# Kernel optimization log

Hardware: AMD Instinct MI355X
Metric: run time of the kernel (lower is better)

Reference implementation:

```python
import jax, jax.numpy as jnp
import numpy as np

B, D = 16, 8192
CH = 32
N_BLOCKS = 24
DILATIONS = [2 ** i for i in range(8)] * 3  # 3 stacks of 8 layers


def _causal_conv(x, W, b, dilation):
    # x: (B, Cin, L); W: (Cout, Cin, K). Causal = left-pad (K-1)*dilation only,
    # which equals torch's symmetric-pad-then-slice-right trick.
    pad = (W.shape[-1] - 1) * dilation
    y = jax.lax.conv_general_dilated(
        x, W, window_strides=(1,), padding=[(pad, 0)],
        rhs_dilation=(dilation,), dimension_numbers=('NCH', 'OIH', 'NCH'))
    return y + b[None, :, None]


def setup_inputs() -> dict:
    key = jax.random.key(0)
    ks = jax.random.split(key, 13)
    s = 0.1  # keep activations in a sane range
    return {
        'x': jax.random.normal(ks[0], (B, D), jnp.float32),
        'W0': jax.random.normal(ks[1], (CH, 1, 2), jnp.float32) * s,
        'b0': jax.random.normal(ks[2], (CH,), jnp.float32) * s,
        'Wd': jax.random.normal(ks[3], (N_BLOCKS, 2 * CH, CH, 2), jnp.float32) * s,
        'bd': jax.random.normal(ks[4], (N_BLOCKS, 2 * CH), jnp.float32) * s,
        'W1': jax.random.normal(ks[5], (N_BLOCKS, CH, CH), jnp.float32) * s,
        'b1': jax.random.normal(ks[6], (N_BLOCKS, CH), jnp.float32) * s,
        'Wf': jax.random.normal(ks[7], (CH, CH), jnp.float32) * s,
        'bf': jax.random.normal(ks[8], (CH,), jnp.float32) * s,
        'fW1': jax.random.normal(ks[9], (64, CH * 4), jnp.float32) * s,
        'fb1': jax.random.normal(ks[10], (64,), jnp.float32) * s,
        'fW2': jax.random.normal(ks[11], (10, 64), jnp.float32) * s,
        'fb2': jax.random.normal(ks[12], (10,), jnp.float32) * s,
    }


def reference(x, W0, b0, Wd, bd, W1, b1, Wf, bf, fW1, fb1, fW2, fb2):
    h = _causal_conv(x[:, None, :], W0, b0, 1)  # (B, 32, L)
    skip_sum = jnp.zeros_like(h)
    for i, dil in enumerate(DILATIONS):
        z = _causal_conv(h, Wd[i], bd[i], dil)          # (B, 64, L)
        f, g = jnp.split(z, 2, axis=1)
        gated = jnp.tanh(f) * jax.nn.sigmoid(g)          # (B, 32, L)
        skip = jnp.einsum('oc,bcl->bol', W1[i], gated) + b1[i][None, :, None]
        h = h + skip                                     # residual (dropout = eval identity)
        skip_sum = skip_sum + skip                       # sum of stacked skips
    y = jax.nn.relu(skip_sum)
    y = jnp.einsum('oc,bcl->bol', Wf, y) + bf[None, :, None]
    y = jax.nn.relu(y)
    # AdaptiveMaxPool1d(4): L divisible by 4 -> max over contiguous chunks
    Bc, C, L = y.shape
    y = y.reshape(Bc, C, 4, L // 4).max(axis=-1)         # (B, 32, 4)
    y = y.reshape(Bc, C * 4)
    y = jax.nn.relu(y @ fW1.T + fb1)
    return y @ fW2.T + fb2
```

## Files before the change

kernel.cpp:

```cpp
#include <hip/hip_runtime.h>
#include <hip/hip_bf16.h>

#define BATCH 16
#define SEQ 8192
#define CH 32
#define NB 24

typedef __attribute__((ext_vector_type(8))) short short8;
typedef __attribute__((ext_vector_type(4))) short short4v;
typedef __attribute__((ext_vector_type(4))) float f32x4;

#define LROW 36

__device__ __forceinline__ unsigned short f2bf(float x) {
    __hip_bfloat16 b = __float2bfloat16(x);
    unsigned short u;
    __builtin_memcpy(&u, &b, 2);
    return u;
}
__device__ __forceinline__ float bf2f(unsigned short h) {
    return __uint_as_float(((unsigned int)h) << 16);
}
__device__ __forceinline__ float rcp_fast(float x) { return __builtin_amdgcn_rcpf(x); }

__device__ __forceinline__ float gate_fn(float f, float g) {
    float ef = __expf(-2.0f * fabsf(f));
    float eg = __expf(-g);
    float num = 1.0f - ef;
    float den = (1.0f + ef) * (1.0f + eg);
    return copysignf(num * rcp_fast(den), f);
}

__device__ __forceinline__ void split2(float v, unsigned short& h, unsigned short& l) {
    h = f2bf(v);
    l = f2bf(v - bf2f(h));
}

__global__ __launch_bounds__(64) void k_prep(const float* __restrict__ Wd,
                                             const float* __restrict__ bd,
                                             const float* __restrict__ W1,
                                             const float* __restrict__ b1,
                                             unsigned short* __restrict__ stream,
                                             float* __restrict__ pooled) {
    int i = blockIdx.x;
    int l = threadIdx.x;
    int p = l & 15, h4 = l >> 4;
    const float* wd  = Wd + (size_t)i * 64 * 64;
    const float* w1  = W1 + (size_t)i * 1024;
    const float* bdp = bd + (size_t)i * 64;
    const float* b1p = b1 + (size_t)i * 32;
    unsigned short* out = stream + (size_t)i * (28672 / 2);

    for (int g = blockIdx.x * 64 + l; g < BATCH * CH * 4; g += NB * 64)
        pooled[g] = 0.0f;

    for (int rt = 0; rt < 4; ++rt)
        for (int q = 0; q < 2; ++q) {
            int slot = rt * 2 + q;
            for (int j = 0; j < 8; ++j) {
                int m = 16 * rt + p;
                int k = 32 * q + 8 * h4 + j;
                int c = k & 31, tap = k >> 5;
                float w = wd[m * 64 + c * 2 + tap];
                unsigned short hi = f2bf(w);
                out[(size_t)slot * 512 + l * 8 + j] = hi;
                out[(size_t)(8 + slot) * 512 + l * 8 + j] = f2bf(w - bf2f(hi));
            }
        }
    for (int rt2 = 0; rt2 < 2; ++rt2)
        for (int j = 0; j < 8; ++j) {
            int o = 16 * rt2 + p, c = 8 * h4 + j;
            float w = w1[o * 32 + c];
            unsigned short hi = f2bf(w);
            out[(size_t)(16 + rt2) * 512 + l * 8 + j] = hi;
            out[(size_t)(18 + rt2) * 512 + l * 8 + j] = f2bf(w - bf2f(hi));
        }
    float* outf = (float*)stream + (size_t)i * (28672 / 4);
    for (int rt = 0; rt < 4; ++rt)
        for (int r = 0; r < 4; ++r)
            outf[(size_t)(20 + rt) * 256 + l * 4 + r] = bdp[16 * rt + 4 * h4 + r];
    for (int rt2 = 0; rt2 < 2; ++rt2)
        for (int r = 0; r < 4; ++r)
            outf[(size_t)(24 + rt2) * 256 + l * 4 + r] = b1p[16 * rt2 + 4 * h4 + r];
}

__global__ __launch_bounds__(512, 2) void k_stack(
        const float* __restrict__ hin,
        float* __restrict__ hout,
        const float* __restrict__ x,
        const float* __restrict__ W0,
        const float* __restrict__ b0,
        const float* __restrict__ Wf,
        const float* __restrict__ bf,
        float* __restrict__ pooled,
        const unsigned short* __restrict__ wstream,
        int stack) {
    __shared__ __align__(16) float lh[768 * LROW];
    __shared__ __align__(16) unsigned short gbuf[8][2][2][16][40];
    __shared__ float red[8 * CH];

    int tid = threadIdx.x;
    int lane = tid & 63, wave = tid >> 6;
    int p = lane & 15, h4 = lane >> 4;
    int bb = blockIdx.x >> 4;
    int T0 = (blockIdx.x & 15) * 512;
    bool first = (stack == 0);
    bool last  = (stack == 2);

    const float* pin = hin + (size_t)bb * SEQ * CH;
    float* pout = hout + (size_t)bb * SEQ * CH;
    const float* px = x + (size_t)bb * SEQ;

    const f32x4 zero4 = {0.0f, 0.0f, 0.0f, 0.0f};

    if (first) {
        for (int i = tid; i < 768; i += 512) {
            int t = T0 - 256 + i;
            float* dst = &lh[i * LROW];
            if (t >= 0) {
                float xt = px[t];
                float xm = (t > 0) ? px[t - 1] : 0.0f;
                __align__(16) float hv[CH];
#pragma unroll
                for (int c = 0; c < CH; ++c)
                    hv[c] = W0[c * 2] * xm + W0[c * 2 + 1] * xt + b0[c];
#pragma unroll
                for (int k = 0; k < 8; ++k)
                    *(f32x4*)(dst + 4 * k) = *(const f32x4*)(hv + 4 * k);
            } else {
#pragma unroll
                for (int k = 0; k < 8; ++k)
                    *(f32x4*)(dst + 4 * k) = zero4;
            }
        }
    } else {
        for (int i = tid; i < 768; i += 512) {
            int t = T0 - 256 + i;
            float* dst = &lh[i * LROW];
            if (t >= 0) {
                const float* src = pin + (size_t)t * CH;
#pragma unroll
                for (int k = 0; k < 8; ++k)
                    *(f32x4*)(dst + 4 * k) = *(const f32x4*)(src + 4 * k);
            } else {
#pragma unroll
                for (int k = 0; k < 8; ++k)
                    *(f32x4*)(dst + 4 * k) = zero4;
            }
        }
    }
    __syncthreads();

#pragma unroll 1
    for (int l = 0; l < 8; ++l) {
        int dil = 1 << l;
        const unsigned short* frag = wstream + (size_t)(8 * stack + l) * 14336;
        const short8* fs = (const short8*)frag;
        short8 Ah[4][2], Al[4][2], Sh[2], Sl[2];
#pragma unroll
        for (int rt = 0; rt < 4; ++rt)
#pragma unroll
            for (int q = 0; q < 2; ++q) {
                Ah[rt][q] = fs[(rt * 2 + q) * 64 + lane];
                Al[rt][q] = fs[(8 + rt * 2 + q) * 64 + lane];
            }
#pragma unroll
        for (int rt2 = 0; rt2 < 2; ++rt2) {
            Sh[rt2] = fs[(16 + rt2) * 64 + lane];
            Sl[rt2] = fs[(18 + rt2) * 64 + lane];
        }
        const f32x4* ff = (const f32x4*)frag;
        f32x4 bFG[4], bS[2];
#pragma unroll
        for (int rt = 0; rt < 4; ++rt) bFG[rt] = ff[(20 + rt) * 64 + lane];
#pragma unroll
        for (int rt2 = 0; rt2 < 2; ++rt2) bS[rt2] = ff[(24 + rt2) * 64 + lane];

        f32x4 hnew[6][2];

#pragma unroll
        for (int i = 0; i < 7; ++i) {
            f32x4 acc[4];
            if (i < 6) {
                int tpos = wave * 96 + i * 16 + p;
                int tq = tpos - dil;
                bool ok = (T0 - 256 + tq >= 0);
                int tqc = (tq > 0) ? tq : 0;

                const float* r1 = &lh[tpos * LROW + 8 * h4];
                const float* r0 = &lh[tqc * LROW + 8 * h4];
                f32x4 v1a = *(const f32x4*)r1, v1b = *(const f32x4*)(r1 + 4);
                f32x4 v0a = *(const f32x4*)r0, v0b = *(const f32x4*)(r0 + 4);
                if (!ok) { v0a = zero4; v0b = zero4; }
                short8 bh1, bl1, bh0, bl0;
#pragma unroll
                for (int j = 0; j < 4; ++j) {
                    unsigned short hh, ll;
                    split2(v1a[j], hh, ll); bh1[j] = (short)hh; bl1[j] = (short)ll;
                    split2(v1b[j], hh, ll); bh1[4 + j] = (short)hh; bl1[4 + j] = (short)ll;
                    split2(v0a[j], hh, ll); bh0[j] = (short)hh; bl0[j] = (short)ll;
                    split2(v0b[j], hh, ll); bh0[4 + j] = (short)hh; bl0[4 + j] = (short)ll;
                }
#pragma unroll
                for (int rt = 0; rt < 4; ++rt) {
                    f32x4 a = bFG[rt];
                    a = __builtin_amdgcn_mfma_f32_16x16x32_bf16(Ah[rt][0], bh0, a, 0, 0, 0);
                    a = __builtin_amdgcn_mfma_f32_16x16x32_bf16(Ah[rt][1], bh1, a, 0, 0, 0);
                    a = __builtin_amdgcn_mfma_f32_16x16x32_bf16(Ah[rt][0], bl0, a, 0, 0, 0);
                    a = __builtin_amdgcn_mfma_f32_16x16x32_bf16(Ah[rt][1], bl1, a, 0, 0, 0);
                    a = __builtin_amdgcn_mfma_f32_16x16x32_bf16(Al[rt][0], bh0, a, 0, 0, 0);
                    a = __builtin_amdgcn_mfma_f32_16x16x32_bf16(Al[rt][1], bh1, a, 0, 0, 0);
                    acc[rt] = a;
                }
            }

            if (i > 0) {
                asm volatile("s_waitcnt lgkmcnt(0)" ::: "memory");
                int ip = i - 1;
                int tposP = wave * 96 + ip * 16 + p;
                short8 Bgh = *(const short8*)&gbuf[wave][ip & 1][0][p][8 * h4];
                short8 Bgl = *(const short8*)&gbuf[wave][ip & 1][1][p][8 * h4];

                f32x4 sacc[2];
#pragma unroll
                for (int rt2 = 0; rt2 < 2; ++rt2) {
                    f32x4 a = bS[rt2];
                    a = __builtin_amdgcn_mfma_f32_16x16x32_bf16(Sh[rt2], Bgh, a, 0, 0, 0);
                    a = __builtin_amdgcn_mfma_f32_16x16x32_bf16(Sh[rt2], Bgl, a, 0, 0, 0);
                    a = __builtin_amdgcn_mfma_f32_16x16x32_bf16(Sl[rt2], Bgh, a, 0, 0, 0);
                    sacc[rt2] = a;
                }
#pragma unroll
                for (int rt2 = 0; rt2 < 2; ++rt2) {
                    f32x4 hold = *(const f32x4*)&lh[tposP * LROW + 16 * rt2 + 4 * h4];
                    hnew[ip][rt2] = hold + sacc[rt2];
                }
            }

            if (i < 6) {
#pragma unroll
                for (int rt = 0; rt < 2; ++rt) {
                    __align__(8) unsigned short g4h[4], g4l[4];
#pragma unroll
                    for (int r = 0; r < 4; ++r) {
                        float gated = gate_fn(acc[rt][r], acc[rt + 2][r]);
                        split2(gated, g4h[r], g4l[r]);
                    }
                    *(short4v*)&gbuf[wave][i & 1][0][p][16 * rt + 4 * h4] = *(const short4v*)g4h;
                    *(short4v*)&gbuf[wave][i & 1][1][p][16 * rt + 4 * h4] = *(const short4v*)g4l;
                }
            }
        }
        __syncthreads();

#pragma unroll
        for (int s6 = 0; s6 < 6; ++s6) {
            int tpos = wave * 96 + s6 * 16 + p;
#pragma unroll
            for (int rt2 = 0; rt2 < 2; ++rt2)
                *(f32x4*)&lh[tpos * LROW + 16 * rt2 + 4 * h4] = hnew[s6][rt2];
        }
        __syncthreads();
    }

    if (!last) {
        int i = 256 + tid;
        int t = T0 + tid;
        const float* src = &lh[i * LROW];
        float* dst = pout + (size_t)t * CH;
#pragma unroll
        for (int k = 0; k < 8; ++k)
            *(f32x4*)(dst + 4 * k) = *(const f32x4*)(src + 4 * k);
    } else {
        int i = 256 + tid;
        int t = T0 + tid;
        int q = (blockIdx.x & 15) >> 2;
        float xt = px[t];
        float xm = (t > 0) ? px[t - 1] : 0.0f;
        const float* src = &lh[i * LROW];

        float r[CH];
#pragma unroll
        for (int c = 0; c < CH; ++c) {
            float h0 = W0[c * 2] * xm + W0[c * 2 + 1] * xt + b0[c];
            r[c] = fmaxf(src[c] - h0, 0.0f);
        }
        float y[CH];
#pragma unroll 1
        for (int o = 0; o < CH; ++o) {
            const float* w = Wf + o * CH;
            float a0 = bf[o], a1 = 0.0f, a2 = 0.0f, a3 = 0.0f;
#pragma unroll
            for (int c = 0; c < CH; c += 4) {
                a0 += w[c + 0] * r[c + 0];
                a1 += w[c + 1] * r[c + 1];
                a2 += w[c + 2] * r[c + 2];
                a3 += w[c + 3] * r[c + 3];
            }
            y[o] = fmaxf((a0 + a1) + (a2 + a3), 0.0f);
        }
#pragma unroll
        for (int o = 0; o < CH; ++o) {
#pragma unroll
            for (int off = 32; off >= 1; off >>= 1)
                y[o] = fmaxf(y[o], __shfl_xor(y[o], off));
        }
        if (lane == 0) {
#pragma unroll
            for (int o = 0; o < CH; ++o) red[wave * CH + o] = y[o];
        }
        __syncthreads();
        if (tid < CH) {
            float m = red[tid];
#pragma unroll
            for (int w8 = 1; w8 < 8; ++w8) m = fmaxf(m, red[w8 * CH + tid]);
            atomicMax((unsigned int*)&pooled[bb * (CH * 4) + tid * 4 + q],
                      __float_as_uint(m));
        }
    }
}

__global__ __launch_bounds__(1024) void k_final2(const float* __restrict__ pooled,
                                                 const float* __restrict__ fW1,
                                                 const float* __restrict__ fb1,
                                                 const float* __restrict__ fW2,
                                                 const float* __restrict__ fb2,
                                                 float* __restrict__ out) {
    __shared__ float y1[BATCH * 64];
    int tid = threadIdx.x;
    int b = tid >> 6, o = tid & 63;
    float acc = fb1[o];
#pragma unroll
    for (int j = 0; j < 128; ++j) acc += fW1[o * 128 + j] * pooled[b * 128 + j];
    y1[b * 64 + o] = fmaxf(acc, 0.0f);
    __syncthreads();
    if (tid < BATCH * 10) {
        int bb = tid / 10, o2 = tid % 10;
        float a2 = fb2[o2];
#pragma unroll
        for (int j = 0; j < 64; ++j) a2 += fW2[o2 * 64 + j] * y1[bb * 64 + j];
        out[bb * 10 + o2] = a2;
    }
}

extern "C" void kernel_launch(void* const* d_in, const int* in_sizes, int n_in,
                              void* d_out, int out_size, void* d_ws, size_t ws_size,
                              hipStream_t stream) {
    const float* x   = (const float*)d_in[0];
    const float* W0  = (const float*)d_in[1];
    const float* b0  = (const float*)d_in[2];
    const float* Wd  = (const float*)d_in[3];
    const float* bd  = (const float*)d_in[4];
    const float* W1  = (const float*)d_in[5];
    const float* b1  = (const float*)d_in[6];
    const float* Wf  = (const float*)d_in[7];
    const float* bf  = (const float*)d_in[8];
    const float* fW1 = (const float*)d_in[9];
    const float* fb1 = (const float*)d_in[10];
    const float* fW2 = (const float*)d_in[11];
    const float* fb2 = (const float*)d_in[12];
    float* out = (float*)d_out;

    const size_t HS = (size_t)BATCH * SEQ * CH;
    float* bufA = (float*)d_ws;
    float* bufB = bufA + HS;
    unsigned short* wstream = (unsigned short*)(bufB + HS);
    float* pooled = (float*)(wstream + (size_t)NB * 14336);

    k_prep<<<NB, 64, 0, stream>>>(Wd, bd, W1, b1, wstream, pooled);

    k_stack<<<256, 512, 0, stream>>>(bufA, bufB, x, W0, b0, Wf, bf, pooled, wstream, 0);
    k_stack<<<256, 512, 0, stream>>>(bufB, bufA, x, W0, b0, Wf, bf, pooled, wstream, 1);
    k_stack<<<256, 512, 0, stream>>>(bufA, bufA, x, W0, b0, Wf, bf, pooled, wstream, 2);

    k_final2<<<1, 1024, 0, stream>>>(pooled, fW1, fb1, fW2, fb2, out);
}
```

Before: 328.3 us.

## Permute gate weight rows so gated values feed skip MFMA directly from registers

The dilated-conv weight rows are permuted in the prep kernel so that each lane's filter and gate accumulator outputs line up with the B-operand layout the skip 1x1 MFMA expects. The gated bf16 hi/lo values can then be packed straight into the skip MFMA operands. This drops the per-wave LDS gbuf round trip, the lgkmcnt wait and the one-step software pipeline. The prep kernel is also widened to 256 threads, with one wave per row tile. The cost is that MFMA/gate overlap across iterations now relies on the compiler's scheduling rather than the explicit pipeline.

Result: slower. 338.5 us (+3.1%).

```diff
diff --git a/kernel.cpp b/kernel.cpp
--- a/kernel.cpp
+++ b/kernel.cpp
@@ -7,7 +7,6 @@
 #define NB 24
 
 typedef __attribute__((ext_vector_type(8))) short short8;
-typedef __attribute__((ext_vector_type(4))) short short4v;
 typedef __attribute__((ext_vector_type(4))) float f32x4;
 
 #define LROW 36
@@ -36,14 +35,15 @@
     l = f2bf(v - bf2f(h));
 }
 
-__global__ __launch_bounds__(64) void k_prep(const float* __restrict__ Wd,
-                                             const float* __restrict__ bd,
-                                             const float* __restrict__ W1,
-                                             const float* __restrict__ b1,
-                                             unsigned short* __restrict__ stream,
-                                             float* __restrict__ pooled) {
+__global__ __launch_bounds__(256) void k_prep(const float* __restrict__ Wd,
+                                              const float* __restrict__ bd,
+                                              const float* __restrict__ W1,
+                                              const float* __restrict__ b1,
+                                              unsigned short* __restrict__ stream,
+                                              float* __restrict__ pooled) {
     int i = blockIdx.x;
-    int l = threadIdx.x;
+    int tid = threadIdx.x;
+    int l = tid & 63, q4 = tid >> 6;
     int p = l & 15, h4 = l >> 4;
     const float* wd  = Wd + (size_t)i * 64 * 64;
     const float* w1  = W1 + (size_t)i * 1024;
@@ -51,23 +51,28 @@
     const float* b1p = b1 + (size_t)i * 32;
     unsigned short* out = stream + (size_t)i * (28672 / 2);
 
-    for (int g = blockIdx.x * 64 + l; g < BATCH * CH * 4; g += NB * 64)
+    for (int g = blockIdx.x * 256 + tid; g < BATCH * CH * 4; g += NB * 256)
         pooled[g] = 0.0f;
 
-    for (int rt = 0; rt < 4; ++rt)
+    {
+        int rt = q4;
+        int is_g = (rt >= 2) ? 32 : 0;
+        int ch = 8 * (p >> 2) + 4 * (rt & 1) + (p & 3);
+        int row = ch + is_g;
         for (int q = 0; q < 2; ++q) {
             int slot = rt * 2 + q;
             for (int j = 0; j < 8; ++j) {
-                int m = 16 * rt + p;
                 int k = 32 * q + 8 * h4 + j;
                 int c = k & 31, tap = k >> 5;
-                float w = wd[m * 64 + c * 2 + tap];
+                float w = wd[row * 64 + c * 2 + tap];
                 unsigned short hi = f2bf(w);
                 out[(size_t)slot * 512 + l * 8 + j] = hi;
                 out[(size_t)(8 + slot) * 512 + l * 8 + j] = f2bf(w - bf2f(hi));
             }
         }
-    for (int rt2 = 0; rt2 < 2; ++rt2)
+    }
+    if (q4 < 2) {
+        int rt2 = q4;
         for (int j = 0; j < 8; ++j) {
             int o = 16 * rt2 + p, c = 8 * h4 + j;
             float w = w1[o * 32 + c];
@@ -75,13 +80,21 @@
             out[(size_t)(16 + rt2) * 512 + l * 8 + j] = hi;
             out[(size_t)(18 + rt2) * 512 + l * 8 + j] = f2bf(w - bf2f(hi));
         }
+    }
     float* outf = (float*)stream + (size_t)i * (28672 / 4);
-    for (int rt = 0; rt < 4; ++rt)
-        for (int r = 0; r < 4; ++r)
-            outf[(size_t)(20 + rt) * 256 + l * 4 + r] = bdp[16 * rt + 4 * h4 + r];
-    for (int rt2 = 0; rt2 < 2; ++rt2)
-        for (int r = 0; r < 4; ++r)
-            outf[(size_t)(24 + rt2) * 256 + l * 4 + r] = b1p[16 * rt2 + 4 * h4 + r];
+    if (q4 == 2) {
+        for (int rt = 0; rt < 4; ++rt) {
+            int is_g = (rt >= 2) ? 32 : 0;
+            for (int r = 0; r < 4; ++r)
+                outf[(size_t)(20 + rt) * 256 + l * 4 + r] =
+                    bdp[8 * h4 + 4 * (rt & 1) + r + is_g];
+        }
+    }
+    if (q4 == 3) {
+        for (int rt2 = 0; rt2 < 2; ++rt2)
+            for (int r = 0; r < 4; ++r)
+                outf[(size_t)(24 + rt2) * 256 + l * 4 + r] = b1p[16 * rt2 + 4 * h4 + r];
+    }
 }
 
 __global__ __launch_bounds__(512, 2) void k_stack(
@@ -96,7 +109,6 @@
         const unsigned short* __restrict__ wstream,
         int stack) {
     __shared__ __align__(16) float lh[768 * LROW];
-    __shared__ __align__(16) unsigned short gbuf[8][2][2][16][40];
     __shared__ float red[8 * CH];
 
     int tid = threadIdx.x;
@@ -179,76 +191,66 @@
         f32x4 hnew[6][2];
 
 #pragma unroll
-        for (int i = 0; i < 7; ++i) {
+        for (int s6 = 0; s6 < 6; ++s6) {
+            int tpos = wave * 96 + s6 * 16 + p;
+            int tq = tpos - dil;
+            bool ok = (T0 - 256 + tq >= 0);
+            int tqc = (tq > 0) ? tq : 0;
+
+            const float* r1 = &lh[tpos * LROW + 8 * h4];
+            const float* r0 = &lh[tqc * LROW + 8 * h4];
+            f32x4 v1a = *(const f32x4*)r1, v1b = *(const f32x4*)(r1 + 4);
+            f32x4 v0a = *(const f32x4*)r0, v0b = *(const f32x4*)(r0 + 4);
+            if (!ok) { v0a = zero4; v0b = zero4; }
+            short8 bh1, bl1, bh0, bl0;
+#pragma unroll
+            for (int j = 0; j < 4; ++j) {
+                unsigned short hh, ll;
+                split2(v1a[j], hh, ll); bh1[j] = (short)hh; bl1[j] = (short)ll;
+                split2(v1b[j], hh, ll); bh1[4 + j] = (short)hh; bl1[4 + j] = (short)ll;
+                split2(v0a[j], hh, ll); bh0[j] = (short)hh; bl0[j] = (short)ll;
+                split2(v0b[j], hh, ll); bh0[4 + j] = (short)hh; bl0[4 + j] = (short)ll;
+            }
+
             f32x4 acc[4];
-            if (i < 6) {
-                int tpos = wave * 96 + i * 16 + p;
-                int tq = tpos - dil;
-                bool ok = (T0 - 256 + tq >= 0);
-                int tqc = (tq > 0) ? tq : 0;
-
-                const float* r1 = &lh[tpos * LROW + 8 * h4];
-                const float* r0 = &lh[tqc * LROW + 8 * h4];
-                f32x4 v1a = *(const f32x4*)r1, v1b = *(const f32x4*)(r1 + 4);
-                f32x4 v0a = *(const f32x4*)r0, v0b = *(const f32x4*)(r0 + 4);
-                if (!ok) { v0a = zero4; v0b = zero4; }
-                short8 bh1, bl1, bh0, bl0;
-#pragma unroll
-                for (int j = 0; j < 4; ++j) {
+#pragma unroll
+            for (int rt = 0; rt < 4; ++rt) {
+                f32x4 a = bFG[rt];
+                a = __builtin_amdgcn_mfma_f32_16x16x32_bf16(Ah[rt][0], bh0, a, 0, 0, 0);
+                a = __builtin_amdgcn_mfma_f32_16x16x32_bf16(Ah[rt][1], bh1, a, 0, 0, 0);
+                a = __builtin_amdgcn_mfma_f32_16x16x32_bf16(Ah[rt][0], bl0, a, 0, 0, 0);
+                a = __builtin_amdgcn_mfma_f32_16x16x32_bf16(Ah[rt][1], bl1, a, 0, 0, 0);
+                a = __builtin_amdgcn_mfma_f32_16x16x32_bf16(Al[rt][0], bh0, a, 0, 0, 0);
+                a = __builtin_amdgcn_mfma_f32_16x16x32_bf16(Al[rt][1], bh1, a, 0, 0, 0);
+                acc[rt] = a;
+            }
+
+            short8 Bgh, Bgl;
+#pragma unroll
+            for (int rt = 0; rt < 2; ++rt)
+#pragma unroll
+                for (int r = 0; r < 4; ++r) {
+                    float gated = gate_fn(acc[rt][r], acc[rt + 2][r]);
                     unsigned short hh, ll;
-                    split2(v1a[j], hh, ll); bh1[j] = (short)hh; bl1[j] = (short)ll;
-                    split2(v1b[j], hh, ll); bh1[4 + j] = (short)hh; bl1[4 + j] = (short)ll;
-                    split2(v0a[j], hh, ll); bh0[j] = (short)hh; bl0[j] = (short)ll;
-                    split2(v0b[j], hh, ll); bh0[4 + j] = (short)hh; bl0[4 + j] = (short)ll;
+                    split2(gated, hh, ll);
+                    Bgh[4 * rt + r] = (short)hh;
+                    Bgl[4 * rt + r] = (short)ll;
                 }
-#pragma unroll
-                for (int rt = 0; rt < 4; ++rt) {
-                    f32x4 a = bFG[rt];
-                    a = __builtin_amdgcn_mfma_f32_16x16x32_bf16(Ah[rt][0], bh0, a, 0, 0, 0);
-                    a = __builtin_amdgcn_mfma_f32_16x16x32_bf16(Ah[rt][1], bh1, a, 0, 0, 0);
-                    a = __builtin_amdgcn_mfma_f32_16x16x32_bf16(Ah[rt][0], bl0, a, 0, 0, 0);
-                    a = __builtin_amdgcn_mfma_f32_16x16x32_bf16(Ah[rt][1], bl1, a, 0, 0, 0);
-                    a = __builtin_amdgcn_mfma_f32_16x16x32_bf16(Al[rt][0], bh0, a, 0, 0, 0);
-                    a = __builtin_amdgcn_mfma_f32_16x16x32_bf16(Al[rt][1], bh1, a, 0, 0, 0);
-                    acc[rt] = a;
-                }
-            }
-
-            if (i > 0) {
-                asm volatile("s_waitcnt lgkmcnt(0)" ::: "memory");
-                int ip = i - 1;
-                int tposP = wave * 96 + ip * 16 + p;
-                short8 Bgh = *(const short8*)&gbuf[wave][ip & 1][0][p][8 * h4];
-                short8 Bgl = *(const short8*)&gbuf[wave][ip & 1][1][p][8 * h4];
-
-                f32x4 sacc[2];
-#pragma unroll
-                for (int rt2 = 0; rt2 < 2; ++rt2) {
-                    f32x4 a = bS[rt2];
-                    a = __builtin_amdgcn_mfma_f32_16x16x32_bf16(Sh[rt2], Bgh, a, 0, 0, 0);
-                    a = __builtin_amdgcn_mfma_f32_16x16x32_bf16(Sh[rt2], Bgl, a, 0, 0, 0);
-                    a = __builtin_amdgcn_mfma_f32_16x16x32_bf16(Sl[rt2], Bgh, a, 0, 0, 0);
-                    sacc[rt2] = a;
-                }
-#pragma unroll
-                for (int rt2 = 0; rt2 < 2; ++rt2) {
-                    f32x4 hold = *(const f32x4*)&lh[tposP * LROW + 16 * rt2 + 4 * h4];
-                    hnew[ip][rt2] = hold + sacc[rt2];
-                }
-            }
-
-            if (i < 6) {
-#pragma unroll
-                for (int rt = 0; rt < 2; ++rt) {
-                    __align__(8) unsigned short g4h[4], g4l[4];
-#pragma unroll
-                    for (int r = 0; r < 4; ++r) {
-                        float gated = gate_fn(acc[rt][r], acc[rt + 2][r]);
-                        split2(gated, g4h[r], g4l[r]);
-                    }
-                    *(short4v*)&gbuf[wave][i & 1][0][p][16 * rt + 4 * h4] = *(const short4v*)g4h;
-                    *(short4v*)&gbuf[wave][i & 1][1][p][16 * rt + 4 * h4] = *(const short4v*)g4l;
-                }
+
+            f32x4 sacc[2];
+#pragma unroll
+            for (int rt2 = 0; rt2 < 2; ++rt2) {
+                f32x4 a = bS[rt2];
+                a = __builtin_amdgcn_mfma_f32_16x16x32_bf16(Sh[rt2], Bgh, a, 0, 0, 0);
+                a = __builtin_amdgcn_mfma_f32_16x16x32_bf16(Sh[rt2], Bgl, a, 0, 0, 0);
+                a = __builtin_amdgcn_mfma_f32_16x16x32_bf16(Sl[rt2], Bgh, a, 0, 0, 0);
+                sacc[rt2] = a;
+            }
+
+#pragma unroll
+            for (int rt2 = 0; rt2 < 2; ++rt2) {
+                f32x4 hold = *(const f32x4*)&lh[tpos * LROW + 16 * rt2 + 4 * h4];
+                hnew[s6][rt2] = hold + sacc[rt2];
             }
         }
         __syncthreads();
@@ -367,7 +369,7 @@
     unsigned short* wstream = (unsigned short*)(bufB + HS);
     float* pooled = (float*)(wstream + (size_t)NB * 14336);
 
-    k_prep<<<NB, 64, 0, stream>>>(Wd, bd, W1, b1, wstream, pooled);
+    k_prep<<<NB, 256, 0, stream>>>(Wd, bd, W1, b1, wstream, pooled);
 
     k_stack<<<256, 512, 0, stream>>>(bufA, bufB, x, W0, b0, Wf, bf, pooled, wstream, 0);
     k_stack<<<256, 512, 0, stream>>>(bufB, bufA, x, W0, b0, Wf, bf, pooled, wstream, 1);
```
